# Kernel tuning notes

Hardware: AMD Instinct MI355X
Metric: run time of the kernel (lower is better)

The kernel has to match this reference:

```python
import jax, jax.numpy as jnp
import numpy as np

EMBED_DIM = 1024
NUM_HEADS = 16
HEAD_DIM = EMBED_DIM // NUM_HEADS


def setup_inputs() -> dict:
    key = jax.random.key(0)
    ks = jax.random.split(key, 11)
    L, N, E = 2048, 2, EMBED_DIM
    S = 2048
    def xavier(k, shape):
        fan_in, fan_out = shape[1], shape[0]
        limit = float(np.sqrt(6.0 / (fan_in + fan_out)))
        return jax.random.uniform(k, shape, jnp.float32, -limit, limit)
    return {
        "query": jax.random.normal(ks[0], (L, N, E), jnp.float32),
        "key": jax.random.normal(ks[1], (S, N, E), jnp.float32),
        "value": jax.random.normal(ks[2], (S, N, E), jnp.float32),
        "Wq": xavier(ks[3], (E, E)), "bq": jnp.zeros((E,), jnp.float32),
        "Wk": xavier(ks[4], (E, E)), "bk": jnp.zeros((E,), jnp.float32),
        "Wv": xavier(ks[5], (E, E)), "bv": jnp.zeros((E,), jnp.float32),
        "Wo": xavier(ks[6], (E, E)), "bo": jnp.zeros((E,), jnp.float32),
    }


def reference(query, key, value, Wq, bq, Wk, bk, Wv, bv, Wo, bo):
    # query/key/value: [L, N, E] (seq-first, batch_first=False)
    L, N, E = query.shape
    S = key.shape[0]
    H, D = NUM_HEADS, HEAD_DIM
    q = query @ Wq.T + bq   # [L, N, E]
    k = key @ Wk.T + bk     # [S, N, E]
    v = value @ Wv.T + bv   # [S, N, E]
    # [L, N*H, D] -> [N*H, L, D]
    q = q.reshape(L, N * H, D).transpose(1, 0, 2)
    k = k.reshape(S, N * H, D).transpose(1, 0, 2)
    v = v.reshape(S, N * H, D).transpose(1, 0, 2)
    scores = jnp.einsum("bld,bsd->bls", q, k) / jnp.sqrt(jnp.float32(D))  # [N*H, L, S]
    attn = jax.nn.softmax(scores, axis=-1)  # dropout p=0.0 -> identity
    out = jnp.einsum("bls,bsd->bld", attn, v)  # [N*H, L, D]
    out = out.transpose(1, 0, 2).reshape(L, N, E)
    attn_output = out @ Wo.T + bo  # [L, N, E]
    # need_weights=True, average_attn_weights=True
    attn_weights = attn.reshape(N, H, L, S).mean(axis=1)  # [N, L, S]
    return attn_output, attn_weights
```

## Files before the change

kernel.cpp:

```cpp
#include <hip/hip_runtime.h>

#define EDIM 1024
#define LSEQ 2048
#define NBATCH 2
#define NHEADS 16
#define HDIM 64
#define QSCALE 0.18033688011112042f

typedef unsigned short us;
typedef __attribute__((ext_vector_type(8))) short short8;
typedef __attribute__((ext_vector_type(4))) float floatx4;
typedef __attribute__((ext_vector_type(16))) float floatx16;

#define MFMA16(a, b, c) __builtin_amdgcn_mfma_f32_16x16x32_bf16((a), (b), (c), 0, 0, 0)
#define MFMA32(a, b, c) __builtin_amdgcn_mfma_f32_32x32x16_bf16((a), (b), (c), 0, 0, 0)
#define ZERO16 ((floatx16){0.f,0.f,0.f,0.f,0.f,0.f,0.f,0.f,0.f,0.f,0.f,0.f,0.f,0.f,0.f,0.f})

__device__ __forceinline__ us f2bf(float f) {
  unsigned int u = __float_as_uint(f);
  u += 0x7fffu + ((u >> 16) & 1u);
  return (us)(u >> 16);
}

__device__ __forceinline__ void gload16(const void* g, void* l) {
  __builtin_amdgcn_global_load_lds((const __attribute__((address_space(1))) unsigned int*)g,
                                   (__attribute__((address_space(3))) unsigned int*)l, 16, 0, 0);
}

__device__ __forceinline__ unsigned int cvtpk(float lo, float hi_) {
  unsigned int r;
  asm("v_cvt_pk_bf16_f32 %0, %1, %2" : "=v"(r) : "v"(lo), "v"(hi_));
  return r;
}
__device__ __forceinline__ void plswap(unsigned int& a, unsigned int& b) {
  asm("v_permlane32_swap_b32 %0, %1" : "+v"(a), "+v"(b));
}
__device__ __forceinline__ short8 mkfrag(unsigned int a, unsigned int b, unsigned int c,
                                         unsigned int d) {
  union { unsigned int u[4]; short8 v; } x;
  x.u[0] = a; x.u[1] = b; x.u[2] = c; x.u[3] = d;
  return x.v;
}
__device__ __forceinline__ void pack2(const floatx16 p, short8& f0, short8& f1) {
  unsigned int A = cvtpk(p[0], p[1]), B = cvtpk(p[4], p[5]); plswap(A, B);
  unsigned int C = cvtpk(p[2], p[3]), D = cvtpk(p[6], p[7]); plswap(C, D);
  f0 = mkfrag(A, C, B, D);
  unsigned int E = cvtpk(p[8], p[9]), F = cvtpk(p[12], p[13]); plswap(E, F);
  unsigned int G = cvtpk(p[10], p[11]), H = cvtpk(p[14], p[15]); plswap(G, H);
  f1 = mkfrag(E, G, F, H);
}

__global__ void k_f2bf_all(const float* q, const float* k, const float* v,
                           const float* wq, const float* wk, const float* wv, const float* wo,
                           us* dq, us* dk, us* dv, us* dwq, us* dwk, us* dwv, us* dwo) {
  const int z = blockIdx.y;
  const float* s; us* d; int n8;
  if (z == 0)      { s = q;  d = dq;  n8 = 524288; }
  else if (z == 1) { s = k;  d = dk;  n8 = 524288; }
  else if (z == 2) { s = v;  d = dv;  n8 = 524288; }
  else if (z == 3) { s = wq; d = dwq; n8 = 131072; }
  else if (z == 4) { s = wk; d = dwk; n8 = 131072; }
  else if (z == 5) { s = wv; d = dwv; n8 = 131072; }
  else             { s = wo; d = dwo; n8 = 131072; }
  int i = blockIdx.x * blockDim.x + threadIdx.x;
  int stride = gridDim.x * blockDim.x;
  for (; i < n8; i += stride) {
    float4 a = ((const float4*)s)[2 * i];
    float4 b = ((const float4*)s)[2 * i + 1];
    union { us u[8]; uint4 vv; } o;
    o.u[0] = f2bf(a.x); o.u[1] = f2bf(a.y); o.u[2] = f2bf(a.z); o.u[3] = f2bf(a.w);
    o.u[4] = f2bf(b.x); o.u[5] = f2bf(b.y); o.u[6] = f2bf(b.z); o.u[7] = f2bf(b.w);
    ((uint4*)d)[i] = o.vv;
  }
}

template <int MODE>
__device__ __forceinline__ void gemm_core(us* pool,
                                          const us* __restrict__ A, const us* __restrict__ B,
                                          const float* __restrict__ bias, void* __restrict__ outp,
                                          int row0, int col0, float scale) {
  us* As = pool;
  us* Bs = pool + 4096;
  const int t = threadIdx.x;
  const int w = t >> 6, lane = t & 63;
  const int g = lane >> 4, lr = lane & 15;
  const int wm = (w & 1) * 64, wn = (w >> 1) * 64;
  const int srow = lane >> 2, scol = (lane & 3) * 8;
  const int cA = 2 * w;
  const us* Asrc = A + (size_t)(row0 + cA * 16 + srow) * EDIM + scol;
  const us* Bsrc = B + (size_t)(col0 + cA * 16 + srow) * EDIM + scol;

  floatx4 acc[4][4];
#pragma unroll
  for (int mi = 0; mi < 4; ++mi)
#pragma unroll
    for (int ni = 0; ni < 4; ++ni) acc[mi][ni] = (floatx4){0.f, 0.f, 0.f, 0.f};

  for (int k0 = 0; k0 < EDIM; k0 += 32) {
    gload16(Asrc + k0, As + cA * 512);
    gload16(Asrc + 16 * EDIM + k0, As + cA * 512 + 512);
    gload16(Bsrc + k0, Bs + cA * 512);
    gload16(Bsrc + 16 * EDIM + k0, Bs + cA * 512 + 512);
    __syncthreads();
    short8 af[4], bfr[4];
#pragma unroll
    for (int mi = 0; mi < 4; ++mi) af[mi] = *(const short8*)&As[(wm + mi * 16 + lr) * 32 + g * 8];
#pragma unroll
    for (int ni = 0; ni < 4; ++ni) bfr[ni] = *(const short8*)&Bs[(wn + ni * 16 + lr) * 32 + g * 8];
#pragma unroll
    for (int mi = 0; mi < 4; ++mi)
#pragma unroll
      for (int ni = 0; ni < 4; ++ni) acc[mi][ni] = MFMA16(af[mi], bfr[ni], acc[mi][ni]);
    __syncthreads();
  }

  if (MODE == 1) {
    us* Ct = pool;
#pragma unroll
    for (int ni = 0; ni < 4; ++ni) {
      const int colloc = wn + ni * 16 + lr;
      const float bv = bias[col0 + colloc];
#pragma unroll
      for (int mi = 0; mi < 4; ++mi) {
        const int b = wm + mi * 16 + 4 * g;
        unsigned int lo = (unsigned int)f2bf(acc[mi][ni][0] + bv) |
                          ((unsigned int)f2bf(acc[mi][ni][2] + bv) << 16);
        unsigned int hi = (unsigned int)f2bf(acc[mi][ni][1] + bv) |
                          ((unsigned int)f2bf(acc[mi][ni][3] + bv) << 16);
        *(unsigned int*)&Ct[colloc * 136 + (b >> 1)] = lo;
        *(unsigned int*)&Ct[colloc * 136 + 64 + (b >> 1)] = hi;
      }
    }
    __syncthreads();
    const int rr = t >> 1, half = t & 1;
    const int c = col0 + rr, h = c >> 6, d = c & 63;
    us* dst = (us*)outp + (((size_t)half * NHEADS + h) * HDIM + d) * LSEQ + (row0 >> 1);
    const us* srcRow = &Ct[rr * 136 + half * 64];
#pragma unroll
    for (int j = 0; j < 8; ++j)
      *(uint4*)(dst + j * 8) = *(const uint4*)(srcRow + j * 8);
  } else {
#pragma unroll
    for (int ni = 0; ni < 4; ++ni) {
      const int col = col0 + wn + ni * 16 + lr;
      const float bv = bias[col];
#pragma unroll
      for (int mi = 0; mi < 4; ++mi) {
#pragma unroll
        for (int i = 0; i < 4; ++i) {
          const int row = row0 + wm + mi * 16 + g * 4 + i;
          const float v = (acc[mi][ni][i] + bv) * scale;
          if (MODE == 2) {
            ((float*)outp)[(size_t)row * EDIM + col] = v;
          } else {
            const int n = row & 1, sq = row >> 1;
            const int h = col >> 6, d = col & 63;
            ((us*)outp)[(((size_t)n * NHEADS + h) * LSEQ + sq) * HDIM + d] = f2bf(v);
          }
        }
      }
    }
  }
}

__global__ __launch_bounds__(256) void k_gemm_qkv(
    const us* __restrict__ Xq, const us* __restrict__ Xk, const us* __restrict__ Xv,
    const us* __restrict__ Wqb, const us* __restrict__ Wkb, const us* __restrict__ Wvb,
    const float* __restrict__ bq, const float* __restrict__ bk, const float* __restrict__ bv,
    us* __restrict__ qo, us* __restrict__ ko, us* __restrict__ vo) {
  __shared__ us pool[17408];
  const int z = blockIdx.z;
  if (z == 0)      gemm_core<0>(pool, Xq, Wqb, bq, qo, blockIdx.x * 128, blockIdx.y * 128, QSCALE);
  else if (z == 1) gemm_core<0>(pool, Xk, Wkb, bk, ko, blockIdx.x * 128, blockIdx.y * 128, 1.0f);
  else             gemm_core<1>(pool, Xv, Wvb, bv, vo, blockIdx.x * 128, blockIdx.y * 128, 1.0f);
}

__global__ __launch_bounds__(256) void k_gemm_o(const us* __restrict__ A, const us* __restrict__ B,
                                                const float* __restrict__ bias, float* __restrict__ out) {
  __shared__ us pool[8192];
  gemm_core<2>(pool, A, B, bias, out, blockIdx.x * 128, blockIdx.y * 128, 1.0f);
}

__global__ __launch_bounds__(256) void k_attn(const us* __restrict__ qb, const us* __restrict__ kb,
                                              const us* __restrict__ vt, float* __restrict__ lgell,
                                              us* __restrict__ O) {
  __shared__ us Ks[2][4096];
  __shared__ us Vs[2][4096];
  __shared__ float elt[4][32];
  const int bh = blockIdx.x;
  const int l0 = blockIdx.y * 128;
  const int t = threadIdx.x, w = t >> 6, lane = t & 63;
  const int ql = lane & 31, hi = lane >> 5;

  short8 qf[4];
  {
    const us* qptr = qb + ((size_t)bh * LSEQ + l0 + w * 32 + ql) * HDIM + hi * 8;
#pragma unroll
    for (int dt = 0; dt < 4; ++dt) qf[dt] = *(const short8*)(qptr + dt * 16);
  }

  int off0[4], off1[4];
#pragma unroll
  for (int j = 0; j < 4; ++j) {
    off0[j] = ql * 64 + (((2 * j + hi) ^ (ql & 7)) << 3);
    off1[j] = (32 + ql) * 64 + (((2 * j + hi) ^ (ql & 7)) << 3);
  }

  const int j0 = 2 * w, j1 = 2 * w + 1;
  const int srA = lane >> 3;
  const int scA = ((lane & 7) ^ (lane >> 3)) * 8;
  const us* Kbase = kb + (size_t)bh * LSEQ * HDIM;
  const us* Vbase = vt + (size_t)bh * HDIM * LSEQ;
  const us* Ksrc0 = Kbase + (j0 * 8 + srA) * HDIM + scA;
  const us* Ksrc1 = Kbase + (j1 * 8 + srA) * HDIM + scA;
  const us* Vsrc0 = Vbase + (size_t)(j0 * 8 + srA) * LSEQ + scA;
  const us* Vsrc1 = Vbase + (size_t)(j1 * 8 + srA) * LSEQ + scA;

  floatx16 oacc0 = ZERO16, oacc1 = ZERO16;
  float ellacc = 0.f;

  gload16(Ksrc0, &Ks[0][j0 * 512]); gload16(Ksrc1, &Ks[0][j1 * 512]);
  gload16(Vsrc0, &Vs[0][j0 * 512]); gload16(Vsrc1, &Vs[0][j1 * 512]);
  __syncthreads();

  for (int it = 0; it < 32; ++it) {
    const int cur = it & 1;
    if (it < 31) {
      const int so = (it + 1) * 64;
      us* Kn = Ks[cur ^ 1]; us* Vn = Vs[cur ^ 1];
      gload16(Ksrc0 + so * HDIM, Kn + j0 * 512);
      gload16(Ksrc1 + so * HDIM, Kn + j1 * 512);
      gload16(Vsrc0 + so, Vn + j0 * 512);
      gload16(Vsrc1 + so, Vn + j1 * 512);
    }
    const us* Kc = Ks[cur];
    const us* Vc = Vs[cur];

    floatx16 acc0 = ZERO16, acc1 = ZERO16;
#pragma unroll
    for (int dt = 0; dt < 4; ++dt) {
      acc0 = MFMA32(*(const short8*)&Kc[off0[dt]], qf[dt], acc0);
      acc1 = MFMA32(*(const short8*)&Kc[off1[dt]], qf[dt], acc1);
    }
#pragma unroll
    for (int r = 0; r < 16; ++r) {
      acc0[r] = __builtin_amdgcn_exp2f(acc0[r]); ellacc += acc0[r];
      acc1[r] = __builtin_amdgcn_exp2f(acc1[r]); ellacc += acc1[r];
    }
    short8 pa0, pa1, pa2, pa3;
    pack2(acc0, pa0, pa1);
    pack2(acc1, pa2, pa3);
#pragma unroll
    for (int dt2 = 0; dt2 < 2; ++dt2) {
      floatx16& oa = dt2 ? oacc1 : oacc0;
      const int* off = dt2 ? off1 : off0;
      oa = MFMA32(pa0, *(const short8*)&Vc[off[0]], oa);
      oa = MFMA32(pa1, *(const short8*)&Vc[off[1]], oa);
      oa = MFMA32(pa2, *(const short8*)&Vc[off[2]], oa);
      oa = MFMA32(pa3, *(const short8*)&Vc[off[3]], oa);
    }
    __syncthreads();
  }

  const float elltot = ellacc + __shfl_xor(ellacc, 32);
  if (lane < 32) {
    elt[w][lane] = 1.0f / elltot;
    lgell[(size_t)bh * LSEQ + l0 + w * 32 + lane] = __builtin_amdgcn_logf(elltot);
  }
  const int n = bh >> 4, hh = bh & 15;
  us* obase = O + (size_t)n * EDIM + (size_t)hh * HDIM;
#pragma unroll
  for (int r = 0; r < 16; ++r) {
    const int q = (r & 3) + 8 * (r >> 2) + 4 * hi;
    const float rl = elt[w][q];
    const size_t l = l0 + w * 32 + q;
    obase[l * (NBATCH * EDIM) + ql] = f2bf(oacc0[r] * rl);
    obase[l * (NBATCH * EDIM) + 32 + ql] = f2bf(oacc1[r] * rl);
  }
}

__global__ __launch_bounds__(256) void k_weights(const us* __restrict__ qb, const us* __restrict__ kb,
                                                 const float* __restrict__ lgell,
                                                 float* __restrict__ Wout) {
  __shared__ us Ks[2][4096];
  __shared__ float lgt[4][32];
  const int l0 = blockIdx.x * 128;
  const int s0 = blockIdx.y * 64;
  const int n = blockIdx.z;
  const int t = threadIdx.x, w = t >> 6, lane = t & 63;
  const int ql = lane & 31, hi = lane >> 5;
  const int j0 = 2 * w, j1 = 2 * w + 1;
  const int srA = lane >> 3;
  const int scA = ((lane & 7) ^ (lane >> 3)) * 8;
  const us* Kb0 = kb + ((size_t)(n * NHEADS) * LSEQ + s0 + j0 * 8 + srA) * HDIM + scA;
  const us* Kb1 = kb + ((size_t)(n * NHEADS) * LSEQ + s0 + j1 * 8 + srA) * HDIM + scA;

  int off0[4], off1[4];
#pragma unroll
  for (int j = 0; j < 4; ++j) {
    off0[j] = ql * 64 + (((2 * j + hi) ^ (ql & 7)) << 3);
    off1[j] = (32 + ql) * 64 + (((2 * j + hi) ^ (ql & 7)) << 3);
  }

  floatx16 wacc0 = ZERO16, wacc1 = ZERO16;

  gload16(Kb0, &Ks[0][j0 * 512]); gload16(Kb1, &Ks[0][j1 * 512]);

  short8 qc[4], qn[4];
  float lgc, lgn = 0.f;
  {
    const us* qptr = qb + ((size_t)(n * NHEADS) * LSEQ + l0 + w * 32 + ql) * HDIM + hi * 8;
#pragma unroll
    for (int dt = 0; dt < 4; ++dt) qc[dt] = *(const short8*)(qptr + dt * 16);
  }
  lgc = (lane < 32) ? lgell[(size_t)(n * NHEADS) * LSEQ + l0 + w * 32 + lane] : 0.f;
  __syncthreads();

  for (int h = 0; h < NHEADS; ++h) {
    const int cur = h & 1;
    if (h < NHEADS - 1) {
      us* Kn2 = Ks[cur ^ 1];
      gload16(Kb0 + (size_t)(h + 1) * LSEQ * HDIM, Kn2 + j0 * 512);
      gload16(Kb1 + (size_t)(h + 1) * LSEQ * HDIM, Kn2 + j1 * 512);
      const us* qptr = qb + ((size_t)(n * NHEADS + h + 1) * LSEQ + l0 + w * 32 + ql) * HDIM + hi * 8;
#pragma unroll
      for (int dt = 0; dt < 4; ++dt) qn[dt] = *(const short8*)(qptr + dt * 16);
      if (lane < 32) lgn = lgell[(size_t)(n * NHEADS + h + 1) * LSEQ + l0 + w * 32 + lane];
    }
    if (lane < 32) lgt[w][lane] = lgc;
    const us* Kc = Ks[cur];
    floatx16 acc0 = ZERO16, acc1 = ZERO16;
#pragma unroll
    for (int dt = 0; dt < 4; ++dt) {
      acc0 = MFMA32(qc[dt], *(const short8*)&Kc[off0[dt]], acc0);
      acc1 = MFMA32(qc[dt], *(const short8*)&Kc[off1[dt]], acc1);
    }
#pragma unroll
    for (int r = 0; r < 16; ++r) {
      const float lg = lgt[w][(r & 3) + 8 * (r >> 2) + 4 * hi];
      wacc0[r] += __builtin_amdgcn_exp2f(acc0[r] - lg);
      wacc1[r] += __builtin_amdgcn_exp2f(acc1[r] - lg);
    }
#pragma unroll
    for (int dt = 0; dt < 4; ++dt) qc[dt] = qn[dt];
    lgc = lgn;
    __syncthreads();
  }

  float* wbase = Wout + (size_t)n * LSEQ * LSEQ + (size_t)s0;
#pragma unroll
  for (int r = 0; r < 16; ++r) {
    const int q = (r & 3) + 8 * (r >> 2) + 4 * hi;
    const size_t row = (size_t)(l0 + w * 32 + q) * LSEQ;
    wbase[row + ql] = wacc0[r] * 0.0625f;
    wbase[row + 32 + ql] = wacc1[r] * 0.0625f;
  }
}

extern "C" void kernel_launch(void* const* d_in, const int* in_sizes, int n_in,
                              void* d_out, int out_size, void* d_ws, size_t ws_size,
                              hipStream_t stream) {
  const float* query = (const float*)d_in[0];
  const float* key   = (const float*)d_in[1];
  const float* value = (const float*)d_in[2];
  const float* Wq = (const float*)d_in[3]; const float* bq = (const float*)d_in[4];
  const float* Wk = (const float*)d_in[5]; const float* bk = (const float*)d_in[6];
  const float* Wv = (const float*)d_in[7]; const float* bv = (const float*)d_in[8];
  const float* Wo = (const float*)d_in[9]; const float* bo = (const float*)d_in[10];

  const size_t MB = 1u << 20;
  char* ws = (char*)d_ws;
  us* Xq  = (us*)(ws + 0 * MB);
  us* Xk  = (us*)(ws + 8 * MB);
  us* Xv  = (us*)(ws + 16 * MB);
  us* Wqb = (us*)(ws + 24 * MB);
  us* Wkb = (us*)(ws + 26 * MB);
  us* Wvb = (us*)(ws + 28 * MB);
  us* Wob = (us*)(ws + 30 * MB);
  us* qbuf = (us*)(ws + 32 * MB);
  us* kbuf = (us*)(ws + 40 * MB);
  us* Vt   = (us*)(ws + 48 * MB);
  us* Obuf = (us*)(ws + 56 * MB);
  float* lgell = (float*)(ws + 64 * MB);

  k_f2bf_all<<<dim3(256, 7), 256, 0, stream>>>(query, key, value, Wq, Wk, Wv, Wo,
                                               Xq, Xk, Xv, Wqb, Wkb, Wvb, Wob);

  k_gemm_qkv<<<dim3(32, 8, 3), 256, 0, stream>>>(Xq, Xk, Xv, Wqb, Wkb, Wvb, bq, bk, bv,
                                                 qbuf, kbuf, Vt);

  k_attn<<<dim3(32, 16), 256, 0, stream>>>(qbuf, kbuf, Vt, lgell, Obuf);

  k_gemm_o<<<dim3(32, 8), 256, 0, stream>>>(Obuf, Wob, bo, (float*)d_out);
  k_weights<<<dim3(16, 32, 2), 256, 0, stream>>>(qbuf, kbuf, lgell, (float*)d_out + 4194304);
}
```

Before: 177.4 us.

## Retile attention-weights kernel to 64 rows per wave with per-lane reciprocal normalizer

Each wave in k_weights now covers 64 query rows instead of 32, so every K fragment read from shared memory feeds twice as many MFMAs. The MFMA operands are swapped so each lane owns a fixed query row. That lets it apply a per-lane reciprocal row sum (now written by k_attn instead of a log-sum) by multiplying, replacing the shared-memory lookup and subtract of the old code. The block count is halved, launch bounds are tightened, and stores become per-row contiguous runs instead of lane-coalesced columns. In exchange, register pressure rises, exp2 of unshifted scores could overflow for large logits, and the store pattern changes.

Result: faster. 173.3 us (-2.3%).

```diff
diff --git a/kernel.cpp b/kernel.cpp
--- a/kernel.cpp
+++ b/kernel.cpp
@@ -182,7 +182,7 @@
 }
 
 __global__ __launch_bounds__(256) void k_attn(const us* __restrict__ qb, const us* __restrict__ kb,
-                                              const us* __restrict__ vt, float* __restrict__ lgell,
+                                              const us* __restrict__ vt, float* __restrict__ rell,
                                               us* __restrict__ O) {
   __shared__ us Ks[2][4096];
   __shared__ us Vs[2][4096];
@@ -264,8 +264,9 @@
 
   const float elltot = ellacc + __shfl_xor(ellacc, 32);
   if (lane < 32) {
-    elt[w][lane] = 1.0f / elltot;
-    lgell[(size_t)bh * LSEQ + l0 + w * 32 + lane] = __builtin_amdgcn_logf(elltot);
+    const float r0 = 1.0f / elltot;
+    elt[w][lane] = r0;
+    rell[(size_t)bh * LSEQ + l0 + w * 32 + lane] = r0;
   }
   const int n = bh >> 4, hh = bh & 15;
   us* obase = O + (size_t)n * EDIM + (size_t)hh * HDIM;
@@ -279,16 +280,16 @@
   }
 }
 
-__global__ __launch_bounds__(256) void k_weights(const us* __restrict__ qb, const us* __restrict__ kb,
-                                                 const float* __restrict__ lgell,
-                                                 float* __restrict__ Wout) {
+__global__ __launch_bounds__(256, 2) void k_weights(const us* __restrict__ qb, const us* __restrict__ kb,
+                                                    const float* __restrict__ rell,
+                                                    float* __restrict__ Wout) {
   __shared__ us Ks[2][4096];
-  __shared__ float lgt[4][32];
-  const int l0 = blockIdx.x * 128;
+  const int l0 = blockIdx.x * 256;
   const int s0 = blockIdx.y * 64;
   const int n = blockIdx.z;
   const int t = threadIdx.x, w = t >> 6, lane = t & 63;
   const int ql = lane & 31, hi = lane >> 5;
+  const int lbase = l0 + w * 64;
   const int j0 = 2 * w, j1 = 2 * w + 1;
   const int srA = lane >> 3;
   const int scA = ((lane & 7) ^ (lane >> 3)) * 8;
@@ -302,58 +303,91 @@
     off1[j] = (32 + ql) * 64 + (((2 * j + hi) ^ (ql & 7)) << 3);
   }
 
-  floatx16 wacc0 = ZERO16, wacc1 = ZERO16;
+  floatx16 wa00 = ZERO16, wa01 = ZERO16, wa10 = ZERO16, wa11 = ZERO16;
 
   gload16(Kb0, &Ks[0][j0 * 512]); gload16(Kb1, &Ks[0][j1 * 512]);
 
-  short8 qc[4], qn[4];
-  float lgc, lgn = 0.f;
+  short8 qc0[4], qc1[4];
+  float rlc0, rlc1;
   {
-    const us* qptr = qb + ((size_t)(n * NHEADS) * LSEQ + l0 + w * 32 + ql) * HDIM + hi * 8;
-#pragma unroll
-    for (int dt = 0; dt < 4; ++dt) qc[dt] = *(const short8*)(qptr + dt * 16);
-  }
-  lgc = (lane < 32) ? lgell[(size_t)(n * NHEADS) * LSEQ + l0 + w * 32 + lane] : 0.f;
+    const us* qp0 = qb + ((size_t)(n * NHEADS) * LSEQ + lbase + ql) * HDIM + hi * 8;
+    const us* qp1 = qp0 + 32 * HDIM;
+#pragma unroll
+    for (int dt = 0; dt < 4; ++dt) {
+      qc0[dt] = *(const short8*)(qp0 + dt * 16);
+      qc1[dt] = *(const short8*)(qp1 + dt * 16);
+    }
+    rlc0 = rell[(size_t)(n * NHEADS) * LSEQ + lbase + ql];
+    rlc1 = rell[(size_t)(n * NHEADS) * LSEQ + lbase + 32 + ql];
+  }
   __syncthreads();
 
   for (int h = 0; h < NHEADS; ++h) {
     const int cur = h & 1;
+    short8 qn0[4], qn1[4];
+    float rln0 = 0.f, rln1 = 0.f;
     if (h < NHEADS - 1) {
       us* Kn2 = Ks[cur ^ 1];
       gload16(Kb0 + (size_t)(h + 1) * LSEQ * HDIM, Kn2 + j0 * 512);
       gload16(Kb1 + (size_t)(h + 1) * LSEQ * HDIM, Kn2 + j1 * 512);
-      const us* qptr = qb + ((size_t)(n * NHEADS + h + 1) * LSEQ + l0 + w * 32 + ql) * HDIM + hi * 8;
-#pragma unroll
-      for (int dt = 0; dt < 4; ++dt) qn[dt] = *(const short8*)(qptr + dt * 16);
-      if (lane < 32) lgn = lgell[(size_t)(n * NHEADS + h + 1) * LSEQ + l0 + w * 32 + lane];
-    }
-    if (lane < 32) lgt[w][lane] = lgc;
+      const us* qp0 = qb + ((size_t)(n * NHEADS + h + 1) * LSEQ + lbase + ql) * HDIM + hi * 8;
+      const us* qp1 = qp0 + 32 * HDIM;
+#pragma unroll
+      for (int dt = 0; dt < 4; ++dt) {
+        qn0[dt] = *(const short8*)(qp0 + dt * 16);
+        qn1[dt] = *(const short8*)(qp1 + dt * 16);
+      }
+      rln0 = rell[(size_t)(n * NHEADS + h + 1) * LSEQ + lbase + ql];
+      rln1 = rell[(size_t)(n * NHEADS + h + 1) * LSEQ + lbase + 32 + ql];
+    }
     const us* Kc = Ks[cur];
-    floatx16 acc0 = ZERO16, acc1 = ZERO16;
+    short8 kf0[4], kf1[4];
 #pragma unroll
     for (int dt = 0; dt < 4; ++dt) {
-      acc0 = MFMA32(qc[dt], *(const short8*)&Kc[off0[dt]], acc0);
-      acc1 = MFMA32(qc[dt], *(const short8*)&Kc[off1[dt]], acc1);
-    }
-#pragma unroll
-    for (int r = 0; r < 16; ++r) {
-      const float lg = lgt[w][(r & 3) + 8 * (r >> 2) + 4 * hi];
-      wacc0[r] += __builtin_amdgcn_exp2f(acc0[r] - lg);
-      wacc1[r] += __builtin_amdgcn_exp2f(acc1[r] - lg);
-    }
-#pragma unroll
-    for (int dt = 0; dt < 4; ++dt) qc[dt] = qn[dt];
-    lgc = lgn;
+      kf0[dt] = *(const short8*)&Kc[off0[dt]];
+      kf1[dt] = *(const short8*)&Kc[off1[dt]];
+    }
+    {
+      floatx16 aA = ZERO16, aB = ZERO16;
+#pragma unroll
+      for (int dt = 0; dt < 4; ++dt) {
+        aA = MFMA32(kf0[dt], qc0[dt], aA);
+        aB = MFMA32(kf1[dt], qc0[dt], aB);
+      }
+#pragma unroll
+      for (int r = 0; r < 16; ++r) {
+        wa00[r] += __builtin_amdgcn_exp2f(aA[r]) * rlc0;
+        wa01[r] += __builtin_amdgcn_exp2f(aB[r]) * rlc0;
+      }
+    }
+    {
+      floatx16 cA = ZERO16, cB = ZERO16;
+#pragma unroll
+      for (int dt = 0; dt < 4; ++dt) {
+        cA = MFMA32(kf0[dt], qc1[dt], cA);
+        cB = MFMA32(kf1[dt], qc1[dt], cB);
+      }
+#pragma unroll
+      for (int r = 0; r < 16; ++r) {
+        wa10[r] += __builtin_amdgcn_exp2f(cA[r]) * rlc1;
+        wa11[r] += __builtin_amdgcn_exp2f(cB[r]) * rlc1;
+      }
+    }
+#pragma unroll
+    for (int dt = 0; dt < 4; ++dt) { qc0[dt] = qn0[dt]; qc1[dt] = qn1[dt]; }
+    rlc0 = rln0; rlc1 = rln1;
     __syncthreads();
   }
 
-  float* wbase = Wout + (size_t)n * LSEQ * LSEQ + (size_t)s0;
+  float* wb0 = Wout + (size_t)n * LSEQ * LSEQ + (size_t)(lbase + ql) * LSEQ + s0;
+  float* wb1 = Wout + (size_t)n * LSEQ * LSEQ + (size_t)(lbase + 32 + ql) * LSEQ + s0;
 #pragma unroll
   for (int r = 0; r < 16; ++r) {
-    const int q = (r & 3) + 8 * (r >> 2) + 4 * hi;
-    const size_t row = (size_t)(l0 + w * 32 + q) * LSEQ;
-    wbase[row + ql] = wacc0[r] * 0.0625f;
-    wbase[row + 32 + ql] = wacc1[r] * 0.0625f;
+    const int cr = (r & 3) + 8 * (r >> 2) + 4 * hi;
+    wb0[cr] = wa00[r] * 0.0625f;
+    wb0[32 + cr] = wa01[r] * 0.0625f;
+    wb1[cr] = wa10[r] * 0.0625f;
+    wb1[32 + cr] = wa11[r] * 0.0625f;
   }
 }
 
@@ -381,7 +415,7 @@
   us* kbuf = (us*)(ws + 40 * MB);
   us* Vt   = (us*)(ws + 48 * MB);
   us* Obuf = (us*)(ws + 56 * MB);
-  float* lgell = (float*)(ws + 64 * MB);
+  float* rell = (float*)(ws + 64 * MB);
 
   k_f2bf_all<<<dim3(256, 7), 256, 0, stream>>>(query, key, value, Wq, Wk, Wv, Wo,
                                                Xq, Xk, Xv, Wqb, Wkb, Wvb, Wob);
@@ -389,8 +423,8 @@
   k_gemm_qkv<<<dim3(32, 8, 3), 256, 0, stream>>>(Xq, Xk, Xv, Wqb, Wkb, Wvb, bq, bk, bv,
                                                  qbuf, kbuf, Vt);
 
-  k_attn<<<dim3(32, 16), 256, 0, stream>>>(qbuf, kbuf, Vt, lgell, Obuf);
+  k_attn<<<dim3(32, 16), 256, 0, stream>>>(qbuf, kbuf, Vt, rell, Obuf);
 
   k_gemm_o<<<dim3(32, 8), 256, 0, stream>>>(Obuf, Wob, bo, (float*)d_out);
-  k_weights<<<dim3(16, 32, 2), 256, 0, stream>>>(qbuf, kbuf, lgell, (float*)d_out + 4194304);
-}
+  k_weights<<<dim3(8, 32, 2), 256, 0, stream>>>(qbuf, kbuf, rell, (float*)d_out + 4194304);
+}
```
